# Optimization experiments

Measured on AMD Instinct MI355X. Metric: run time of the kernel, lower is better.

The kernel has to match this reference:

```python
import jax, jax.numpy as jnp
import numpy as np

N_COMPRESS = 512
N_EXPAND_QK = 512
N_EXPAND_V = 512
TOPK_C, TOPK_QK, TOPK_V = 8, 4, 6


def setup_inputs() -> dict:
    key = jax.random.key(0)
    k1, k2, k3 = jax.random.split(key, 3)
    B, S, D, DS = 4, 4096, 2048, 64
    N = N_COMPRESS + N_EXPAND_QK + N_EXPAND_V
    x = jax.random.normal(k1, (B, S, D), dtype=jnp.float32)
    importance = jax.random.uniform(k2, (B, S), dtype=jnp.float32)
    W_proj = jax.random.normal(k3, (D, DS), dtype=jnp.float32) * (1.0 / np.sqrt(D))
    b_proj = jnp.zeros((DS,), dtype=jnp.float32)
    neuron_emb = jax.random.normal(jax.random.fold_in(key, 7), (N, DS), dtype=jnp.float32) * 0.02
    return {"x": x, "importance": importance, "W_proj": W_proj, "b_proj": b_proj, "neuron_emb": neuron_emb}


def _topk_sparsify(w, k):
    # w: [B, N]; keep top-k per row, zero the rest, renormalize (matches torch scatter path)
    vals, idx = jax.lax.top_k(w, k)
    B = w.shape[0]
    sparse = jnp.zeros_like(w).at[jnp.arange(B)[:, None], idx].set(vals)
    return sparse / (sparse.sum(axis=-1, keepdims=True) + 1e-8)


def reference(x, importance, W_proj, b_proj, neuron_emb):
    # token projection into unified neuron space
    h = x @ W_proj + b_proj                              # [B, S, d_space]
    emb_n = neuron_emb / jnp.maximum(
        jnp.linalg.norm(neuron_emb, axis=-1, keepdims=True), 1e-12)
    all_logits = jnp.einsum('bsd,nd->bsn', h, emb_n)     # [B, S, N_total]

    c_end = N_COMPRESS
    qk_end = N_COMPRESS + N_EXPAND_QK
    compress_pref = jax.nn.softmax(all_logits[..., :c_end], axis=-1)
    pref_QK = jax.nn.softmax(all_logits[..., c_end:qk_end], axis=-1)  # Q and K share logits (eval mode)
    pref_V = jax.nn.softmax(all_logits[..., qk_end:], axis=-1)

    # importance-weighted pooling over the sequence
    dense_C = jnp.einsum('bs,bsn->bn', importance, compress_pref)
    dense_QK = jnp.einsum('bs,bsn->bn', importance, pref_QK)
    dense_V = jnp.einsum('bs,bsn->bn', importance, pref_V)

    w_C = _topk_sparsify(dense_C, TOPK_C)
    w_Q = _topk_sparsify(dense_QK, TOPK_QK)
    w_K = _topk_sparsify(dense_QK, TOPK_QK)
    w_V = _topk_sparsify(dense_V, TOPK_V)
    return jnp.stack([w_C, w_Q, w_K, w_V], axis=0)       # [4, B, N_group]
```

## Files before the change

kernel.cpp:

```cpp
#include <hip/hip_runtime.h>

#define NTOT 1536
#define DD 2048
#define BB 4
#define SS 4096
#define NBB 42
#define TPB 98
#define NTILE 7

typedef __attribute__((ext_vector_type(8))) short bf16x8;
typedef __attribute__((ext_vector_type(4))) float f32x4;

__device__ __forceinline__ void split1(float v, unsigned short& hi, unsigned short& lo) {
  unsigned u = __float_as_uint(v);
  hi = (unsigned short)(u >> 16);
  float hf = __uint_as_float(u & 0xffff0000u);
  float r = v - hf;
  lo = (unsigned short)(__float_as_uint(r) >> 16);
}

__device__ __forceinline__ void gload16(const void* g, void* lds) {
  __builtin_amdgcn_global_load_lds(
      (const __attribute__((address_space(1))) unsigned int*)g,
      (__attribute__((address_space(3))) unsigned int*)lds, 16, 0, 0);
}

__global__ __launch_bounds__(256) void k_prep(const float* __restrict__ emb,
                                              const float* __restrict__ W,
                                              short* __restrict__ eH,
                                              short* __restrict__ eL,
                                              short* __restrict__ imgH,
                                              short* __restrict__ imgL) {
  int bid = blockIdx.x;
  if (bid < 384) {
    int wave = threadIdx.x >> 6;
    int lane = threadIdx.x & 63;
    int n = bid * 4 + wave;
    float v = emb[n * 64 + lane];
    float ss = v * v;
#pragma unroll
    for (int off = 32; off; off >>= 1) ss += __shfl_xor(ss, off, 64);
    float nrm = fmaxf(sqrtf(ss), 1e-12f);
    float nv = v / nrm;
    unsigned short hi, lo;
    split1(nv, hi, lo);
    eH[n * 64 + lane] = (short)hi;
    eL[n * 64 + lane] = (short)lo;
  } else {
    int kt = bid - 384;
    for (int idx = threadIdx.x; idx < 4096; idx += 256) {
      int n = idx & 63;
      int q = idx >> 6;
      int p = q >> 3;
      int e = q & 7;
      int s = p ^ (n & 7);
      int k = kt * 64 + s * 8 + e;
      float v = W[k * 64 + n];
      unsigned short hi, lo;
      split1(v, hi, lo);
      int flat = kt * 4096 + n * 64 + p * 8 + e;
      imgH[flat] = (short)hi;
      imgL[flat] = (short)lo;
    }
  }
}

__global__ __launch_bounds__(256, 2) void k_proj(const float* __restrict__ x,
                                                 const float* __restrict__ imgHf,
                                                 const float* __restrict__ imgLf,
                                                 const float* __restrict__ bias,
                                                 short* __restrict__ hH,
                                                 short* __restrict__ hL) {
  __shared__ float XAs[2][2048];
  __shared__ short BHs[2][4096];
  __shared__ short BLs[2][4096];

  int tid = threadIdx.x;
  int w = tid >> 6;
  int l = tid & 63;
  size_t t0 = (size_t)blockIdx.x * 32;

  int th = (w & 1) * 16;
  int nh = (w >> 1) * 32;

  f32x4 acc[2];
#pragma unroll
  for (int i = 0; i < 2; ++i) acc[i] = (f32x4){0.f, 0.f, 0.f, 0.f};

  const float4* imgH4 = (const float4*)imgHf;
  const float4* imgL4 = (const float4*)imgLf;

  size_t xoff[2];
  int xdst[2];
  int ioff[2];
  int bdst[2];
#pragma unroll
  for (int c = 0; c < 2; ++c) {
    int tok = c * 16 + w * 4 + (l >> 4);
    int s = (l & 15) ^ (tok & 7);
    xoff[c] = (t0 + tok) * DD + s * 4;
    xdst[c] = tok * 64 + (l & 15) * 4;
    ioff[c] = c * 256 + tid;
    bdst[c] = (c * 256 + tid) * 8;
  }

#define STAGE(DB, KT)                                                        \
  {                                                                          \
    _Pragma("unroll") for (int c = 0; c < 2; ++c) {                          \
      gload16(x + xoff[c] + (KT) * 64, &XAs[DB][xdst[c]]);                   \
      gload16(imgH4 + (KT) * 512 + ioff[c], &BHs[DB][bdst[c]]);              \
      gload16(imgL4 + (KT) * 512 + ioff[c], &BLs[DB][bdst[c]]);              \
    }                                                                        \
  }

#define COMPUTE(DB)                                                                \
  {                                                                                \
    int row = th + (l & 15);                                                       \
    _Pragma("unroll") for (int ks = 0; ks < 2; ++ks) {                             \
      int s0 = ks * 8 + (l >> 4) * 2;                                              \
      float4 xa = *(const float4*)(&XAs[DB][row * 64 + ((s0 ^ (row & 7)) << 2)]);  \
      float4 xb = *(const float4*)(&XAs[DB][row * 64 + (((s0 + 1) ^ (row & 7)) << 2)]); \
      bf16x8 ahi, alo;                                                             \
      {                                                                            \
        float v[8] = {xa.x, xa.y, xa.z, xa.w, xb.x, xb.y, xb.z, xb.w};             \
        _Pragma("unroll") for (int i = 0; i < 8; ++i) {                            \
          unsigned u = __float_as_uint(v[i]);                                      \
          ahi[i] = (short)(u >> 16);                                               \
          float hf = __uint_as_float(u & 0xffff0000u);                             \
          float r = v[i] - hf;                                                     \
          alo[i] = (short)(__float_as_uint(r) >> 16);                              \
        }                                                                          \
      }                                                                            \
      _Pragma("unroll") for (int nf = 0; nf < 2; ++nf) {                           \
        int n = nh + nf * 16 + (l & 15);                                           \
        int p = (ks * 4 + (l >> 4)) ^ (n & 7);                                     \
        bf16x8 bh = *(const bf16x8*)(&BHs[DB][n * 64 + p * 8]);                    \
        bf16x8 bl = *(const bf16x8*)(&BLs[DB][n * 64 + p * 8]);                    \
        acc[nf] = __builtin_amdgcn_mfma_f32_16x16x32_bf16(ahi, bh, acc[nf], 0, 0, 0); \
        acc[nf] = __builtin_amdgcn_mfma_f32_16x16x32_bf16(alo, bh, acc[nf], 0, 0, 0); \
        acc[nf] = __builtin_amdgcn_mfma_f32_16x16x32_bf16(ahi, bl, acc[nf], 0, 0, 0); \
      }                                                                            \
    }                                                                              \
  }

  STAGE(0, 0);
  STAGE(1, 1);

  int db = 0;
#pragma unroll 1
  for (int kt = 0; kt < 32; ++kt) {
    if (kt < 31) {
      asm volatile("s_waitcnt vmcnt(6)" ::: "memory");
    } else {
      asm volatile("s_waitcnt vmcnt(0)" ::: "memory");
    }
    __builtin_amdgcn_sched_barrier(0);
    __builtin_amdgcn_s_barrier();
    __builtin_amdgcn_sched_barrier(0);
    COMPUTE(db);
    __builtin_amdgcn_sched_barrier(0);
    __builtin_amdgcn_s_barrier();
    __builtin_amdgcn_sched_barrier(0);
    if (kt < 30) STAGE(db, kt + 2);
    db ^= 1;
  }

#pragma unroll
  for (int nf = 0; nf < 2; ++nf) {
    int n = nh + nf * 16 + (l & 15);
    float bv = bias[n];
#pragma unroll
    for (int j = 0; j < 4; ++j) {
      size_t tok = t0 + th + (l >> 4) * 4 + j;
      float v = acc[nf][j] + bv;
      unsigned short hi, lo;
      split1(v, hi, lo);
      hH[tok * 64 + n] = (short)hi;
      hL[tok * 64 + n] = (short)lo;
    }
  }
#undef STAGE
#undef COMPUTE
}

__global__ __launch_bounds__(512, 4) void k_pref(const short* __restrict__ hH,
                                                 const short* __restrict__ hL,
                                                 const short* __restrict__ eH,
                                                 const short* __restrict__ eL,
                                                 const float* __restrict__ imp,
                                                 float* __restrict__ partials) {
  int bid = blockIdx.x;
  int g = bid / (BB * NBB);
  int rem = bid % (BB * NBB);
  int b = rem / NBB;
  int nb = rem % NBB;
  int tid = threadIdx.x;
  int w = tid >> 6;
  int l = tid & 63;
  int col = l & 15;
  int q = l >> 4;

  __shared__ short BLs[4 * 2 * 512 * 8];
  __shared__ float zred[2][8][16];

  bf16x8 BH[4][2];
  {
    const short* eHg = eH + ((size_t)(g * 512 + w * 64 + col)) * 64 + q * 8;
    const short* eLg = eL + ((size_t)(g * 512 + w * 64 + col)) * 64 + q * 8;
#pragma unroll
    for (int nf = 0; nf < 4; ++nf) {
#pragma unroll
      for (int ks = 0; ks < 2; ++ks) {
        BH[nf][ks] = *(const bf16x8*)(eHg + nf * 1024 + ks * 32);
        bf16x8 blv = *(const bf16x8*)(eLg + nf * 1024 + ks * 32);
        *(bf16x8*)(&BLs[((nf * 2 + ks) * 512 + tid) * 8]) = blv;
      }
    }
  }
  __syncthreads();

  int s0 = nb * TPB;
  int slim = s0 + TPB; if (slim > SS) slim = SS;
  float wsum[4] = {0.f, 0.f, 0.f, 0.f};
  int par = 0;

#pragma unroll 1
  for (int tile = 0; tile < NTILE; ++tile) {
    int tbase = s0 + tile * 16;
    int arow = tbase + col; if (arow > SS - 1) arow = SS - 1;
    size_t hoff = ((size_t)b * SS + arow) * 64;
    bf16x8 AH0 = *(const bf16x8*)(hH + hoff + q * 8);
    bf16x8 AH1 = *(const bf16x8*)(hH + hoff + 32 + q * 8);
    bf16x8 AL0 = *(const bf16x8*)(hL + hoff + q * 8);
    bf16x8 AL1 = *(const bf16x8*)(hL + hoff + 32 + q * 8);

    f32x4 acc[4];
#pragma unroll
    for (int nf = 0; nf < 4; ++nf) acc[nf] = (f32x4){0.f, 0.f, 0.f, 0.f};
#pragma unroll
    for (int nf = 0; nf < 4; ++nf) {
      bf16x8 bl0 = *(const bf16x8*)(&BLs[((nf * 2 + 0) * 512 + tid) * 8]);
      bf16x8 bl1 = *(const bf16x8*)(&BLs[((nf * 2 + 1) * 512 + tid) * 8]);
      acc[nf] = __builtin_amdgcn_mfma_f32_16x16x32_bf16(AH0, BH[nf][0], acc[nf], 0, 0, 0);
      acc[nf] = __builtin_amdgcn_mfma_f32_16x16x32_bf16(AL0, BH[nf][0], acc[nf], 0, 0, 0);
      acc[nf] = __builtin_amdgcn_mfma_f32_16x16x32_bf16(AH0, bl0, acc[nf], 0, 0, 0);
      acc[nf] = __builtin_amdgcn_mfma_f32_16x16x32_bf16(AH1, BH[nf][1], acc[nf], 0, 0, 0);
      acc[nf] = __builtin_amdgcn_mfma_f32_16x16x32_bf16(AL1, BH[nf][1], acc[nf], 0, 0, 0);
      acc[nf] = __builtin_amdgcn_mfma_f32_16x16x32_bf16(AH1, bl1, acc[nf], 0, 0, 0);
    }

    float zp[4];
#pragma unroll
    for (int j = 0; j < 4; ++j) {
      zp[j] = __expf(acc[0][j]) + __expf(acc[1][j]) +
              __expf(acc[2][j]) + __expf(acc[3][j]);
    }
#pragma unroll
    for (int off = 1; off <= 8; off <<= 1) {
#pragma unroll
      for (int j = 0; j < 4; ++j) zp[j] += __shfl_xor(zp[j], off, 64);
    }
    float zw = (col == 0) ? zp[0] : (col == 1) ? zp[1] : (col == 2) ? zp[2] : zp[3];
    if (col < 4) zred[par][w][q * 4 + col] = zw;
    __syncthreads();
    float r0, r1, r2, r3;
    {
#pragma unroll
      for (int j = 0; j < 4; ++j) {
        int t16 = q * 4 + j;
        float Z = 0.f;
#pragma unroll
        for (int ww = 0; ww < 8; ++ww) Z += zred[par][ww][t16];
        int s = tbase + t16;
        float iv = (s < slim) ? imp[(size_t)b * SS + s] : 0.f;
        float r = iv / Z;
        if (j == 0) r0 = r; else if (j == 1) r1 = r; else if (j == 2) r2 = r; else r3 = r;
      }
    }
#pragma unroll
    for (int nf = 0; nf < 4; ++nf) {
      wsum[nf] += __expf(acc[nf][0]) * r0 + __expf(acc[nf][1]) * r1 +
                  __expf(acc[nf][2]) * r2 + __expf(acc[nf][3]) * r3;
    }
    par ^= 1;
  }

#pragma unroll
  for (int nf = 0; nf < 4; ++nf) {
    wsum[nf] += __shfl_xor(wsum[nf], 16, 64);
    wsum[nf] += __shfl_xor(wsum[nf], 32, 64);
  }
  if (q == 0) {
    size_t base = ((size_t)(g * BB + b) * NBB + nb) * 512 + w * 64;
#pragma unroll
    for (int nf = 0; nf < 4; ++nf) partials[base + nf * 16 + col] = wsum[nf];
  }
}

__global__ __launch_bounds__(512) void k_topk(const float* __restrict__ partials,
                                              float* __restrict__ out) {
  int g = blockIdx.x >> 2;
  int b = blockIdx.x & 3;
  int tid = threadIdx.x;
  int wave = tid >> 6, lane = tid & 63;

  __shared__ float lv[8][8];
  __shared__ int li[8][8];

  float d0 = 0.f, d1 = 0.f, d2 = 0.f, d3 = 0.f;
  const float* p = partials + (size_t)(g * BB + b) * NBB * 512 + tid;
  int nb = 0;
  for (; nb + 4 <= NBB; nb += 4) {
    d0 += p[(nb + 0) * 512];
    d1 += p[(nb + 1) * 512];
    d2 += p[(nb + 2) * 512];
    d3 += p[(nb + 3) * 512];
  }
  for (; nb < NBB; ++nb) d0 += p[nb * 512];
  float dense = (d0 + d1) + (d2 + d3);

  int K = (g == 0) ? 8 : (g == 1) ? 4 : 6;
  float val = dense;
  float ssum = 0.f;
  int sel = 0;
  for (int it = 0; it < K; ++it) {
    float v = val;
    int idx = tid;
#pragma unroll
    for (int off = 32; off; off >>= 1) {
      float ov = __shfl_xor(v, off, 64);
      int oi = __shfl_xor(idx, off, 64);
      if (ov > v || (ov == v && oi < idx)) { v = ov; idx = oi; }
    }
    if (lane == 0) { lv[wave][0] = v; li[wave][0] = idx; }
    __syncthreads();
    float mv = lv[0][0];
    int mi = li[0][0];
#pragma unroll
    for (int ww = 1; ww < 8; ++ww) {
      float wv2 = lv[ww][0];
      int wi = li[ww][0];
      if (wv2 > mv || (wv2 == mv && wi < mi)) { mv = wv2; mi = wi; }
    }
    ssum += mv;
    if (tid == mi) { sel = 1; val = -3.0e38f; }
    __syncthreads();
  }
  float o = sel ? dense / (ssum + 1e-8f) : 0.f;
  int row = (g == 0) ? 0 : (g == 1) ? 1 : 3;
  out[((size_t)row * BB + b) * 512 + tid] = o;
  if (g == 1) out[((size_t)2 * BB + b) * 512 + tid] = o;
}

extern "C" void kernel_launch(void* const* d_in, const int* in_sizes, int n_in,
                              void* d_out, int out_size, void* d_ws, size_t ws_size,
                              hipStream_t stream) {
  const float* x    = (const float*)d_in[0];
  const float* imp  = (const float*)d_in[1];
  const float* W    = (const float*)d_in[2];
  const float* bias = (const float*)d_in[3];
  const float* emb  = (const float*)d_in[4];
  float* out = (float*)d_out;

  char* ws = (char*)d_ws;
  short* imgH     = (short*)(ws + 0);
  short* imgL     = (short*)(ws + 262144);
  short* eH       = (short*)(ws + 524288);
  short* eL       = (short*)(ws + 720896);
  short* hH       = (short*)(ws + 917504);
  short* hL       = (short*)(ws + 3014656);
  float* partials = (float*)(ws + 5111808);

  hipLaunchKernelGGL(k_prep, dim3(416), dim3(256), 0, stream, emb, W, eH, eL, imgH, imgL);
  hipLaunchKernelGGL(k_proj, dim3(512), dim3(256), 0, stream,
                     x, (const float*)imgH, (const float*)imgL, bias, hH, hL);
  hipLaunchKernelGGL(k_pref, dim3(3 * BB * NBB), dim3(512), 0, stream,
                     hH, hL, eH, eL, imp, partials);
  hipLaunchKernelGGL(k_topk, dim3(12), dim3(512), 0, stream, partials, out);
}
```

Before: 91.14 us.

## Fuse all four stages into one cooperative kernel with grid syncs

Replaces four separate kernel launches with one cooperative persistent kernel of 512 blocks of 512 threads, using grid.sync between prep, projection, preference and top-k stages, with a shared-memory union. The projection stage is retiled to 64 tokens per block and 8 waves, and its hand-tuned vmcnt-based double-buffer pipeline becomes a simpler stage-then-__syncthreads loop. The pref stage caches exp values instead of recomputing them. This aims to remove launch gaps, but risks lower occupancy, grid-sync overhead and weaker load/compute overlap in the projection; if cooperative launch fails it falls back to four launches.

```diff
diff --git a/kernel.cpp b/kernel.cpp
--- a/kernel.cpp
+++ b/kernel.cpp
@@ -1,4 +1,7 @@
 #include <hip/hip_runtime.h>
+#include <hip/hip_cooperative_groups.h>
+
+namespace cg = cooperative_groups;
 
 #define NTOT 1536
 #define DD 2048
@@ -11,6 +14,11 @@
 typedef __attribute__((ext_vector_type(8))) short bf16x8;
 typedef __attribute__((ext_vector_type(4))) float f32x4;
 
+struct ProjS { float XAs[2][4096]; short BHs[2][4096]; short BLs[2][4096]; };
+struct PrefS { short BLs[4 * 2 * 512 * 8]; float zred[2][8][16]; };
+struct TopkS { float lv[8]; int li[8]; };
+union SMemU { ProjS proj; PrefS pref; TopkS topk; };
+
 __device__ __forceinline__ void split1(float v, unsigned short& hi, unsigned short& lo) {
   unsigned u = __float_as_uint(v);
   hi = (unsigned short)(u >> 16);
@@ -25,18 +33,15 @@
       (__attribute__((address_space(3))) unsigned int*)lds, 16, 0, 0);
 }
 
-__global__ __launch_bounds__(256) void k_prep(const float* __restrict__ emb,
-                                              const float* __restrict__ W,
-                                              short* __restrict__ eH,
-                                              short* __restrict__ eL,
-                                              short* __restrict__ imgH,
-                                              short* __restrict__ imgL) {
-  int bid = blockIdx.x;
-  if (bid < 384) {
-    int wave = threadIdx.x >> 6;
-    int lane = threadIdx.x & 63;
-    int n = bid * 4 + wave;
-    float v = emb[n * 64 + lane];
+__device__ __forceinline__ void st_prep(int bid, int tid,
+                                        const float* __restrict__ emb,
+                                        const float* __restrict__ W,
+                                        short* __restrict__ eH, short* __restrict__ eL,
+                                        short* __restrict__ imgH, short* __restrict__ imgL) {
+  int w = tid >> 6, l = tid & 63;
+  if (bid < 192) {
+    int n = bid * 8 + w;
+    float v = emb[n * 64 + l];
     float ss = v * v;
 #pragma unroll
     for (int off = 32; off; off >>= 1) ss += __shfl_xor(ss, off, 64);
@@ -44,11 +49,11 @@
     float nv = v / nrm;
     unsigned short hi, lo;
     split1(nv, hi, lo);
-    eH[n * 64 + lane] = (short)hi;
-    eL[n * 64 + lane] = (short)lo;
-  } else {
-    int kt = bid - 384;
-    for (int idx = threadIdx.x; idx < 4096; idx += 256) {
+    eH[n * 64 + l] = (short)hi;
+    eL[n * 64 + l] = (short)lo;
+  } else if (bid < 224) {
+    int kt = bid - 192;
+    for (int idx = tid; idx < 4096; idx += 512) {
       int n = idx & 63;
       int q = idx >> 6;
       int p = q >> 3;
@@ -65,52 +70,43 @@
   }
 }
 
-__global__ __launch_bounds__(256, 2) void k_proj(const float* __restrict__ x,
-                                                 const float* __restrict__ imgHf,
-                                                 const float* __restrict__ imgLf,
-                                                 const float* __restrict__ bias,
-                                                 short* __restrict__ hH,
-                                                 short* __restrict__ hL) {
-  __shared__ float XAs[2][2048];
-  __shared__ short BHs[2][4096];
-  __shared__ short BLs[2][4096];
-
-  int tid = threadIdx.x;
-  int w = tid >> 6;
-  int l = tid & 63;
-  size_t t0 = (size_t)blockIdx.x * 32;
-
-  int th = (w & 1) * 16;
-  int nh = (w >> 1) * 32;
+__device__ __forceinline__ void st_proj(int bid, int tid,
+                                        const float* __restrict__ x,
+                                        const short* __restrict__ imgHs,
+                                        const short* __restrict__ imgLs,
+                                        const float* __restrict__ bias,
+                                        short* __restrict__ hH, short* __restrict__ hL,
+                                        ProjS& s) {
+  int w = tid >> 6, l = tid & 63;
+  size_t t0 = (size_t)bid * 64;
+  int th = (w & 3) * 16;
+  int nh = (w >> 2) * 32;
+
+  const float4* imgH4 = (const float4*)imgHs;
+  const float4* imgL4 = (const float4*)imgLs;
 
   f32x4 acc[2];
 #pragma unroll
   for (int i = 0; i < 2; ++i) acc[i] = (f32x4){0.f, 0.f, 0.f, 0.f};
-
-  const float4* imgH4 = (const float4*)imgHf;
-  const float4* imgL4 = (const float4*)imgLf;
 
   size_t xoff[2];
   int xdst[2];
-  int ioff[2];
-  int bdst[2];
 #pragma unroll
   for (int c = 0; c < 2; ++c) {
-    int tok = c * 16 + w * 4 + (l >> 4);
-    int s = (l & 15) ^ (tok & 7);
-    xoff[c] = (t0 + tok) * DD + s * 4;
-    xdst[c] = tok * 64 + (l & 15) * 4;
-    ioff[c] = c * 256 + tid;
-    bdst[c] = (c * 256 + tid) * 8;
-  }
+    int tok = c * 32 + (tid >> 4);
+    int sl = (tid & 15) ^ (tok & 7);
+    xoff[c] = (t0 + tok) * DD + sl * 4;
+    xdst[c] = tok * 64 + (tid & 15) * 4;
+  }
+  int ioff = tid;
+  int bdst = tid * 8;
 
 #define STAGE(DB, KT)                                                        \
   {                                                                          \
-    _Pragma("unroll") for (int c = 0; c < 2; ++c) {                          \
-      gload16(x + xoff[c] + (KT) * 64, &XAs[DB][xdst[c]]);                   \
-      gload16(imgH4 + (KT) * 512 + ioff[c], &BHs[DB][bdst[c]]);              \
-      gload16(imgL4 + (KT) * 512 + ioff[c], &BLs[DB][bdst[c]]);              \
-    }                                                                        \
+    gload16(x + xoff[0] + (KT) * 64, &s.XAs[DB][xdst[0]]);                   \
+    gload16(x + xoff[1] + (KT) * 64, &s.XAs[DB][xdst[1]]);                   \
+    gload16(imgH4 + (KT) * 512 + ioff, &s.BHs[DB][bdst]);                    \
+    gload16(imgL4 + (KT) * 512 + ioff, &s.BLs[DB][bdst]);                    \
   }
 
 #define COMPUTE(DB)                                                                \
@@ -118,8 +114,8 @@
     int row = th + (l & 15);                                                       \
     _Pragma("unroll") for (int ks = 0; ks < 2; ++ks) {                             \
       int s0 = ks * 8 + (l >> 4) * 2;                                              \
-      float4 xa = *(const float4*)(&XAs[DB][row * 64 + ((s0 ^ (row & 7)) << 2)]);  \
-      float4 xb = *(const float4*)(&XAs[DB][row * 64 + (((s0 + 1) ^ (row & 7)) << 2)]); \
+      float4 xa = *(const float4*)(&s.XAs[DB][row * 64 + ((s0 ^ (row & 7)) << 2)]); \
+      float4 xb = *(const float4*)(&s.XAs[DB][row * 64 + (((s0 + 1) ^ (row & 7)) << 2)]); \
       bf16x8 ahi, alo;                                                             \
       {                                                                            \
         float v[8] = {xa.x, xa.y, xa.z, xa.w, xb.x, xb.y, xb.z, xb.w};             \
@@ -134,8 +130,8 @@
       _Pragma("unroll") for (int nf = 0; nf < 2; ++nf) {                           \
         int n = nh + nf * 16 + (l & 15);                                           \
         int p = (ks * 4 + (l >> 4)) ^ (n & 7);                                     \
-        bf16x8 bh = *(const bf16x8*)(&BHs[DB][n * 64 + p * 8]);                    \
-        bf16x8 bl = *(const bf16x8*)(&BLs[DB][n * 64 + p * 8]);                    \
+        bf16x8 bh = *(const bf16x8*)(&s.BHs[DB][n * 64 + p * 8]);                  \
+        bf16x8 bl = *(const bf16x8*)(&s.BLs[DB][n * 64 + p * 8]);                  \
         acc[nf] = __builtin_amdgcn_mfma_f32_16x16x32_bf16(ahi, bh, acc[nf], 0, 0, 0); \
         acc[nf] = __builtin_amdgcn_mfma_f32_16x16x32_bf16(alo, bh, acc[nf], 0, 0, 0); \
         acc[nf] = __builtin_amdgcn_mfma_f32_16x16x32_bf16(ahi, bl, acc[nf], 0, 0, 0); \
@@ -144,24 +140,14 @@
   }
 
   STAGE(0, 0);
-  STAGE(1, 1);
+  __syncthreads();
 
   int db = 0;
 #pragma unroll 1
   for (int kt = 0; kt < 32; ++kt) {
-    if (kt < 31) {
-      asm volatile("s_waitcnt vmcnt(6)" ::: "memory");
-    } else {
-      asm volatile("s_waitcnt vmcnt(0)" ::: "memory");
-    }
-    __builtin_amdgcn_sched_barrier(0);
-    __builtin_amdgcn_s_barrier();
-    __builtin_amdgcn_sched_barrier(0);
+    if (kt < 31) STAGE(db ^ 1, kt + 1);
     COMPUTE(db);
-    __builtin_amdgcn_sched_barrier(0);
-    __builtin_amdgcn_s_barrier();
-    __builtin_amdgcn_sched_barrier(0);
-    if (kt < 30) STAGE(db, kt + 2);
+    __syncthreads();
     db ^= 1;
   }
 
@@ -183,25 +169,20 @@
 #undef COMPUTE
 }
 
-__global__ __launch_bounds__(512, 4) void k_pref(const short* __restrict__ hH,
-                                                 const short* __restrict__ hL,
-                                                 const short* __restrict__ eH,
-                                                 const short* __restrict__ eL,
-                                                 const float* __restrict__ imp,
-                                                 float* __restrict__ partials) {
-  int bid = blockIdx.x;
+__device__ __forceinline__ void st_pref(int bid, int tid,
+                                        const short* __restrict__ hH,
+                                        const short* __restrict__ hL,
+                                        const short* __restrict__ eH,
+                                        const short* __restrict__ eL,
+                                        const float* __restrict__ imp,
+                                        float* __restrict__ partials,
+                                        PrefS& s) {
   int g = bid / (BB * NBB);
   int rem = bid % (BB * NBB);
   int b = rem / NBB;
   int nb = rem % NBB;
-  int tid = threadIdx.x;
-  int w = tid >> 6;
-  int l = tid & 63;
-  int col = l & 15;
-  int q = l >> 4;
-
-  __shared__ short BLs[4 * 2 * 512 * 8];
-  __shared__ float zred[2][8][16];
+  int w = tid >> 6, l = tid & 63;
+  int col = l & 15, q = l >> 4;
 
   bf16x8 BH[4][2];
   {
@@ -213,7 +194,7 @@
       for (int ks = 0; ks < 2; ++ks) {
         BH[nf][ks] = *(const bf16x8*)(eHg + nf * 1024 + ks * 32);
         bf16x8 blv = *(const bf16x8*)(eLg + nf * 1024 + ks * 32);
-        *(bf16x8*)(&BLs[((nf * 2 + ks) * 512 + tid) * 8]) = blv;
+        *(bf16x8*)(&s.BLs[((nf * 2 + ks) * 512 + tid) * 8]) = blv;
       }
     }
   }
@@ -239,8 +220,8 @@
     for (int nf = 0; nf < 4; ++nf) acc[nf] = (f32x4){0.f, 0.f, 0.f, 0.f};
 #pragma unroll
     for (int nf = 0; nf < 4; ++nf) {
-      bf16x8 bl0 = *(const bf16x8*)(&BLs[((nf * 2 + 0) * 512 + tid) * 8]);
-      bf16x8 bl1 = *(const bf16x8*)(&BLs[((nf * 2 + 1) * 512 + tid) * 8]);
+      bf16x8 bl0 = *(const bf16x8*)(&s.BLs[((nf * 2 + 0) * 512 + tid) * 8]);
+      bf16x8 bl1 = *(const bf16x8*)(&s.BLs[((nf * 2 + 1) * 512 + tid) * 8]);
       acc[nf] = __builtin_amdgcn_mfma_f32_16x16x32_bf16(AH0, BH[nf][0], acc[nf], 0, 0, 0);
       acc[nf] = __builtin_amdgcn_mfma_f32_16x16x32_bf16(AL0, BH[nf][0], acc[nf], 0, 0, 0);
       acc[nf] = __builtin_amdgcn_mfma_f32_16x16x32_bf16(AH0, bl0, acc[nf], 0, 0, 0);
@@ -249,11 +230,14 @@
       acc[nf] = __builtin_amdgcn_mfma_f32_16x16x32_bf16(AH1, bl1, acc[nf], 0, 0, 0);
     }
 
-    float zp[4];
+    float e0[4], e1[4], e2[4], e3[4], zp[4];
 #pragma unroll
     for (int j = 0; j < 4; ++j) {
-      zp[j] = __expf(acc[0][j]) + __expf(acc[1][j]) +
-              __expf(acc[2][j]) + __expf(acc[3][j]);
+      e0[j] = __expf(acc[0][j]);
+      e1[j] = __expf(acc[1][j]);
+      e2[j] = __expf(acc[2][j]);
+      e3[j] = __expf(acc[3][j]);
+      zp[j] = e0[j] + e1[j] + e2[j] + e3[j];
     }
 #pragma unroll
     for (int off = 1; off <= 8; off <<= 1) {
@@ -261,27 +245,24 @@
       for (int j = 0; j < 4; ++j) zp[j] += __shfl_xor(zp[j], off, 64);
     }
     float zw = (col == 0) ? zp[0] : (col == 1) ? zp[1] : (col == 2) ? zp[2] : zp[3];
-    if (col < 4) zred[par][w][q * 4 + col] = zw;
+    if (col < 4) s.zred[par][w][q * 4 + col] = zw;
     __syncthreads();
     float r0, r1, r2, r3;
-    {
-#pragma unroll
-      for (int j = 0; j < 4; ++j) {
-        int t16 = q * 4 + j;
-        float Z = 0.f;
-#pragma unroll
-        for (int ww = 0; ww < 8; ++ww) Z += zred[par][ww][t16];
-        int s = tbase + t16;
-        float iv = (s < slim) ? imp[(size_t)b * SS + s] : 0.f;
-        float r = iv / Z;
-        if (j == 0) r0 = r; else if (j == 1) r1 = r; else if (j == 2) r2 = r; else r3 = r;
-      }
-    }
-#pragma unroll
-    for (int nf = 0; nf < 4; ++nf) {
-      wsum[nf] += __expf(acc[nf][0]) * r0 + __expf(acc[nf][1]) * r1 +
-                  __expf(acc[nf][2]) * r2 + __expf(acc[nf][3]) * r3;
-    }
+#pragma unroll
+    for (int j = 0; j < 4; ++j) {
+      int t16 = q * 4 + j;
+      float Z = 0.f;
+#pragma unroll
+      for (int ww = 0; ww < 8; ++ww) Z += s.zred[par][ww][t16];
+      int ss2 = tbase + t16;
+      float iv = (ss2 < slim) ? imp[(size_t)b * SS + ss2] : 0.f;
+      float r = iv / Z;
+      if (j == 0) r0 = r; else if (j == 1) r1 = r; else if (j == 2) r2 = r; else r3 = r;
+    }
+    wsum[0] += e0[0] * r0 + e0[1] * r1 + e0[2] * r2 + e0[3] * r3;
+    wsum[1] += e1[0] * r0 + e1[1] * r1 + e1[2] * r2 + e1[3] * r3;
+    wsum[2] += e2[0] * r0 + e2[1] * r1 + e2[2] * r2 + e2[3] * r3;
+    wsum[3] += e3[0] * r0 + e3[1] * r1 + e3[2] * r2 + e3[3] * r3;
     par ^= 1;
   }
 
@@ -297,15 +278,12 @@
   }
 }
 
-__global__ __launch_bounds__(512) void k_topk(const float* __restrict__ partials,
-                                              float* __restrict__ out) {
-  int g = blockIdx.x >> 2;
-  int b = blockIdx.x & 3;
-  int tid = threadIdx.x;
+__device__ __forceinline__ void st_topk(int bid, int tid,
+                                        const float* __restrict__ partials,
+                                        float* __restrict__ out, TopkS& s) {
+  int g = bid >> 2;
+  int b = bid & 3;
   int wave = tid >> 6, lane = tid & 63;
-
-  __shared__ float lv[8][8];
-  __shared__ int li[8][8];
 
   float d0 = 0.f, d1 = 0.f, d2 = 0.f, d3 = 0.f;
   const float* p = partials + (size_t)(g * BB + b) * NBB * 512 + tid;
@@ -332,14 +310,14 @@
       int oi = __shfl_xor(idx, off, 64);
       if (ov > v || (ov == v && oi < idx)) { v = ov; idx = oi; }
     }
-    if (lane == 0) { lv[wave][0] = v; li[wave][0] = idx; }
+    if (lane == 0) { s.lv[wave] = v; s.li[wave] = idx; }
     __syncthreads();
-    float mv = lv[0][0];
-    int mi = li[0][0];
+    float mv = s.lv[0];
+    int mi = s.li[0];
 #pragma unroll
     for (int ww = 1; ww < 8; ++ww) {
-      float wv2 = lv[ww][0];
-      int wi = li[ww][0];
+      float wv2 = s.lv[ww];
+      int wi = s.li[ww];
       if (wv2 > mv || (wv2 == mv && wi < mi)) { mv = wv2; mi = wi; }
     }
     ssum += mv;
@@ -350,6 +328,48 @@
   int row = (g == 0) ? 0 : (g == 1) ? 1 : 3;
   out[((size_t)row * BB + b) * 512 + tid] = o;
   if (g == 1) out[((size_t)2 * BB + b) * 512 + tid] = o;
+}
+
+__global__ __launch_bounds__(512, 4) void k_fused(const float* x, const float* imp,
+                                                  const float* W, const float* bias,
+                                                  const float* emb,
+                                                  short* eH, short* eL,
+                                                  short* imgH, short* imgL,
+                                                  short* hH, short* hL,
+                                                  float* partials, float* out) {
+  __shared__ SMemU sm;
+  cg::grid_group grid = cg::this_grid();
+  int bid = blockIdx.x, tid = threadIdx.x;
+
+  st_prep(bid, tid, emb, W, eH, eL, imgH, imgL);
+  grid.sync();
+  if (bid < 256) st_proj(bid, tid, x, imgH, imgL, bias, hH, hL, sm.proj);
+  grid.sync();
+  if (bid < 504) st_pref(bid, tid, hH, hL, eH, eL, imp, partials, sm.pref);
+  grid.sync();
+  if (bid < 12) st_topk(bid, tid, partials, out, sm.topk);
+}
+
+__global__ __launch_bounds__(512, 4) void k_s0(const float* emb, const float* W,
+                                               short* eH, short* eL,
+                                               short* imgH, short* imgL) {
+  st_prep(blockIdx.x, threadIdx.x, emb, W, eH, eL, imgH, imgL);
+}
+__global__ __launch_bounds__(512, 4) void k_s1(const float* x, const short* imgH,
+                                               const short* imgL, const float* bias,
+                                               short* hH, short* hL) {
+  __shared__ ProjS s;
+  st_proj(blockIdx.x, threadIdx.x, x, imgH, imgL, bias, hH, hL, s);
+}
+__global__ __launch_bounds__(512, 4) void k_s2(const short* hH, const short* hL,
+                                               const short* eH, const short* eL,
+                                               const float* imp, float* partials) {
+  __shared__ PrefS s;
+  st_pref(blockIdx.x, threadIdx.x, hH, hL, eH, eL, imp, partials, s);
+}
+__global__ __launch_bounds__(512, 4) void k_s3(const float* partials, float* out) {
+  __shared__ TopkS s;
+  st_topk(blockIdx.x, threadIdx.x, partials, out, s);
 }
 
 extern "C" void kernel_launch(void* const* d_in, const int* in_sizes, int n_in,
@@ -371,10 +391,17 @@
   short* hL       = (short*)(ws + 3014656);
   float* partials = (float*)(ws + 5111808);
 
-  hipLaunchKernelGGL(k_prep, dim3(416), dim3(256), 0, stream, emb, W, eH, eL, imgH, imgL);
-  hipLaunchKernelGGL(k_proj, dim3(512), dim3(256), 0, stream,
-                     x, (const float*)imgH, (const float*)imgL, bias, hH, hL);
-  hipLaunchKernelGGL(k_pref, dim3(3 * BB * NBB), dim3(512), 0, stream,
-                     hH, hL, eH, eL, imp, partials);
-  hipLaunchKernelGGL(k_topk, dim3(12), dim3(512), 0, stream, partials, out);
-}
+  void* kargs[] = {(void*)&x, (void*)&imp, (void*)&W, (void*)&bias, (void*)&emb,
+                   (void*)&eH, (void*)&eL, (void*)&imgH, (void*)&imgL,
+                   (void*)&hH, (void*)&hL, (void*)&partials, (void*)&out};
+  hipError_t err = hipLaunchCooperativeKernel((void*)k_fused, dim3(512), dim3(512),
+                                              kargs, 0, stream);
+  if (err != hipSuccess) {
+    hipLaunchKernelGGL(k_s0, dim3(224), dim3(512), 0, stream, emb, W, eH, eL, imgH, imgL);
+    hipLaunchKernelGGL(k_s1, dim3(256), dim3(512), 0, stream,
+                       x, (const short*)imgH, (const short*)imgL, bias, hH, hL);
+    hipLaunchKernelGGL(k_s2, dim3(504), dim3(512), 0, stream,
+                       hH, hL, eH, eL, imp, partials);
+    hipLaunchKernelGGL(k_s3, dim3(12), dim3(512), 0, stream, partials, out);
+  }
+}
```

After: 255.6 us. +180.4%, slower.

## Fuse top-k into pref kernel via last-block atomic counter; cache exps

Applied to the files above, without the earlier changes.

Removes the separate top-k kernel launch. Each pref block atomically increments a per-(group,batch) counter, and the last block to finish reduces the partials and runs the top-k selection. The counter is reset in the prep kernel. It also computes the exponentials once and reuses them, instead of recomputing them for the weighted sum. The cost is extra fences and atomics in every block, plus a serialized tail done by one block per group.

```diff
diff --git a/kernel.cpp b/kernel.cpp
--- a/kernel.cpp
+++ b/kernel.cpp
@@ -30,8 +30,10 @@
                                               short* __restrict__ eH,
                                               short* __restrict__ eL,
                                               short* __restrict__ imgH,
-                                              short* __restrict__ imgL) {
+                                              short* __restrict__ imgL,
+                                              unsigned* __restrict__ cnt) {
   int bid = blockIdx.x;
+  if (bid == 0 && threadIdx.x < 12) cnt[threadIdx.x] = 0;
   if (bid < 384) {
     int wave = threadIdx.x >> 6;
     int lane = threadIdx.x & 63;
@@ -188,7 +190,9 @@
                                                  const short* __restrict__ eH,
                                                  const short* __restrict__ eL,
                                                  const float* __restrict__ imp,
-                                                 float* __restrict__ partials) {
+                                                 float* __restrict__ partials,
+                                                 unsigned* __restrict__ cnt,
+                                                 float* __restrict__ out) {
   int bid = blockIdx.x;
   int g = bid / (BB * NBB);
   int rem = bid % (BB * NBB);
@@ -202,6 +206,9 @@
 
   __shared__ short BLs[4 * 2 * 512 * 8];
   __shared__ float zred[2][8][16];
+  __shared__ float lv[8];
+  __shared__ int li[8];
+  __shared__ int lastFlag;
 
   bf16x8 BH[4][2];
   {
@@ -249,11 +256,14 @@
       acc[nf] = __builtin_amdgcn_mfma_f32_16x16x32_bf16(AH1, bl1, acc[nf], 0, 0, 0);
     }
 
-    float zp[4];
+    float e0[4], e1[4], e2[4], e3[4], zp[4];
 #pragma unroll
     for (int j = 0; j < 4; ++j) {
-      zp[j] = __expf(acc[0][j]) + __expf(acc[1][j]) +
-              __expf(acc[2][j]) + __expf(acc[3][j]);
+      e0[j] = __expf(acc[0][j]);
+      e1[j] = __expf(acc[1][j]);
+      e2[j] = __expf(acc[2][j]);
+      e3[j] = __expf(acc[3][j]);
+      zp[j] = e0[j] + e1[j] + e2[j] + e3[j];
     }
 #pragma unroll
     for (int off = 1; off <= 8; off <<= 1) {
@@ -264,24 +274,21 @@
     if (col < 4) zred[par][w][q * 4 + col] = zw;
     __syncthreads();
     float r0, r1, r2, r3;
-    {
-#pragma unroll
-      for (int j = 0; j < 4; ++j) {
-        int t16 = q * 4 + j;
-        float Z = 0.f;
-#pragma unroll
-        for (int ww = 0; ww < 8; ++ww) Z += zred[par][ww][t16];
-        int s = tbase + t16;
-        float iv = (s < slim) ? imp[(size_t)b * SS + s] : 0.f;
-        float r = iv / Z;
-        if (j == 0) r0 = r; else if (j == 1) r1 = r; else if (j == 2) r2 = r; else r3 = r;
-      }
-    }
-#pragma unroll
-    for (int nf = 0; nf < 4; ++nf) {
-      wsum[nf] += __expf(acc[nf][0]) * r0 + __expf(acc[nf][1]) * r1 +
-                  __expf(acc[nf][2]) * r2 + __expf(acc[nf][3]) * r3;
-    }
+#pragma unroll
+    for (int j = 0; j < 4; ++j) {
+      int t16 = q * 4 + j;
+      float Z = 0.f;
+#pragma unroll
+      for (int ww = 0; ww < 8; ++ww) Z += zred[par][ww][t16];
+      int s = tbase + t16;
+      float iv = (s < slim) ? imp[(size_t)b * SS + s] : 0.f;
+      float r = iv / Z;
+      if (j == 0) r0 = r; else if (j == 1) r1 = r; else if (j == 2) r2 = r; else r3 = r;
+    }
+    wsum[0] += e0[0] * r0 + e0[1] * r1 + e0[2] * r2 + e0[3] * r3;
+    wsum[1] += e1[0] * r0 + e1[1] * r1 + e1[2] * r2 + e1[3] * r3;
+    wsum[2] += e2[0] * r0 + e2[1] * r1 + e2[2] * r2 + e2[3] * r3;
+    wsum[3] += e3[0] * r0 + e3[1] * r1 + e3[2] * r2 + e3[3] * r3;
     par ^= 1;
   }
 
@@ -295,28 +302,28 @@
 #pragma unroll
     for (int nf = 0; nf < 4; ++nf) partials[base + nf * 16 + col] = wsum[nf];
   }
-}
-
-__global__ __launch_bounds__(512) void k_topk(const float* __restrict__ partials,
-                                              float* __restrict__ out) {
-  int g = blockIdx.x >> 2;
-  int b = blockIdx.x & 3;
-  int tid = threadIdx.x;
+
+  __threadfence();
+  __syncthreads();
+  if (tid == 0) {
+    unsigned old = atomicAdd(&cnt[g * BB + b], 1u);
+    lastFlag = (old == NBB - 1u) ? 1 : 0;
+  }
+  __syncthreads();
+  if (!lastFlag) return;
+  __threadfence();
+
   int wave = tid >> 6, lane = tid & 63;
-
-  __shared__ float lv[8][8];
-  __shared__ int li[8][8];
-
   float d0 = 0.f, d1 = 0.f, d2 = 0.f, d3 = 0.f;
   const float* p = partials + (size_t)(g * BB + b) * NBB * 512 + tid;
-  int nb = 0;
-  for (; nb + 4 <= NBB; nb += 4) {
-    d0 += p[(nb + 0) * 512];
-    d1 += p[(nb + 1) * 512];
-    d2 += p[(nb + 2) * 512];
-    d3 += p[(nb + 3) * 512];
-  }
-  for (; nb < NBB; ++nb) d0 += p[nb * 512];
+  int nb2 = 0;
+  for (; nb2 + 4 <= NBB; nb2 += 4) {
+    d0 += p[(nb2 + 0) * 512];
+    d1 += p[(nb2 + 1) * 512];
+    d2 += p[(nb2 + 2) * 512];
+    d3 += p[(nb2 + 3) * 512];
+  }
+  for (; nb2 < NBB; ++nb2) d0 += p[nb2 * 512];
   float dense = (d0 + d1) + (d2 + d3);
 
   int K = (g == 0) ? 8 : (g == 1) ? 4 : 6;
@@ -332,14 +339,14 @@
       int oi = __shfl_xor(idx, off, 64);
       if (ov > v || (ov == v && oi < idx)) { v = ov; idx = oi; }
     }
-    if (lane == 0) { lv[wave][0] = v; li[wave][0] = idx; }
+    if (lane == 0) { lv[wave] = v; li[wave] = idx; }
     __syncthreads();
-    float mv = lv[0][0];
-    int mi = li[0][0];
+    float mv = lv[0];
+    int mi = li[0];
 #pragma unroll
     for (int ww = 1; ww < 8; ++ww) {
-      float wv2 = lv[ww][0];
-      int wi = li[ww][0];
+      float wv2 = lv[ww];
+      int wi = li[ww];
       if (wv2 > mv || (wv2 == mv && wi < mi)) { mv = wv2; mi = wi; }
     }
     ssum += mv;
@@ -370,11 +377,11 @@
   short* hH       = (short*)(ws + 917504);
   short* hL       = (short*)(ws + 3014656);
   float* partials = (float*)(ws + 5111808);
-
-  hipLaunchKernelGGL(k_prep, dim3(416), dim3(256), 0, stream, emb, W, eH, eL, imgH, imgL);
+  unsigned* cnt   = (unsigned*)(ws + 6144000);
+
+  hipLaunchKernelGGL(k_prep, dim3(416), dim3(256), 0, stream, emb, W, eH, eL, imgH, imgL, cnt);
   hipLaunchKernelGGL(k_proj, dim3(512), dim3(256), 0, stream,
                      x, (const float*)imgH, (const float*)imgL, bias, hH, hL);
   hipLaunchKernelGGL(k_pref, dim3(3 * BB * NBB), dim3(512), 0, stream,
-                     hH, hL, eH, eL, imp, partials);
-  hipLaunchKernelGGL(k_topk, dim3(12), dim3(512), 0, stream, partials, out);
-}
+                     hH, hL, eH, eL, imp, partials, cnt, out);
+}
```

Result: slower. 151.1 us (+65.8%).
